# Performance work log

Measured on AMD Instinct MI355X. Metric: run time of the kernel, lower is better.

## Reference

```python
import jax, jax.numpy as jnp
import numpy as np

N = 50000          # total nodes
N_USER = 40000     # main (user) nodes
E = 400000         # edges per node kind
K = 3              # node kinds (separate graphs)
H = 4              # attention heads
F_IN = 128         # n_units[0]
F_OUT = 64         # n_units[1]
NB_CLASSES = 40
SLOPE = 0.2        # leaky relu negative slope


def setup_inputs() -> dict:
    key = jax.random.key(0)
    ks = jax.random.split(key, 12)
    h = jax.random.normal(ks[0], (N, F_IN), dtype=jnp.float32)
    edge_index = jax.random.randint(ks[1], (K, 2, E), 0, N, dtype=jnp.int32)
    # per-kind SpGATLayer params (bias=False)
    w = jax.random.normal(ks[2], (K, H, F_IN, F_OUT), dtype=jnp.float32) * 0.1
    a_src = jax.random.normal(ks[3], (K, H, F_OUT), dtype=jnp.float32) * 0.1
    a_trg = jax.random.normal(ks[4], (K, H, F_OUT), dtype=jnp.float32) * 0.1
    # AdditiveAttention: w1 (d=F_IN -> d2=F_OUT), w2 (d1=F_OUT -> d2=F_OUT), m (d2 -> 1)
    w1 = jax.random.normal(ks[5], (F_IN, F_OUT), dtype=jnp.float32) * 0.1
    w2 = jax.random.normal(ks[6], (F_OUT, F_OUT), dtype=jnp.float32) * 0.1
    m = jax.random.normal(ks[7], (F_OUT,), dtype=jnp.float32) * 0.1
    # final fc: in = F_OUT*(K+1)
    fc_w = jax.random.normal(ks[8], (F_OUT * (K + 1), NB_CLASSES), dtype=jnp.float32) * 0.1
    fc_b = jnp.zeros((NB_CLASSES,), dtype=jnp.float32)
    return {"h": h, "edge_index": edge_index, "w": w, "a_src": a_src,
            "a_trg": a_trg, "w1": w1, "w2": w2, "m": m,
            "fc_w": fc_w, "fc_b": fc_b}


def _spgat_kind(h, src, trg, wk, ask, atk):
    # h: [N, F_IN], wk: [H, F_IN, F_OUT], ask/atk: [H, F_OUT]
    hp = jnp.einsum('nd,hdf->nhf', h, wk)               # [N, H, F_OUT]
    s = jnp.einsum('nhf,hf->nh', hp, ask)               # [N, H]
    t = jnp.einsum('nhf,hf->nh', hp, atk)               # [N, H]
    e = s[src] + t[trg]                                 # [E, H]
    e = jnp.where(e >= 0, e, SLOPE * e)                 # leaky relu
    e = e - jnp.max(e)                                  # global max shift (as in source)
    exp_e = jnp.exp(e)
    denom = jax.ops.segment_sum(exp_e, trg, num_segments=N)  # [N, H]
    alpha = exp_e / (denom[trg] + 1e-16)                # [E, H]
    msg = hp[src] * alpha[:, :, None]                   # [E, H, F_OUT]
    out = jax.ops.segment_sum(msg, trg, num_segments=N) # [N, H, F_OUT]
    return out.mean(axis=1)                             # [N, F_OUT] (last layer head-mean)


def reference(h, edge_index, w, a_src, a_trg, w1, w2, m, fc_w, fc_b):
    heter = []
    for k in range(K):  # fixed small loop over node kinds
        x = _spgat_kind(h, edge_index[k, 0], edge_index[k, 1],
                        w[k], a_src[k], a_trg[k])
        heter.append(x[:N_USER])
    type_aware = jnp.stack(heter, axis=1)               # [N_USER, K, F_OUT]
    feature = h[:N_USER]                                # [N_USER, F_IN]
    q = jnp.tanh((feature @ w1)[:, None, :] + type_aware @ w2)  # [N_USER, K, F_OUT]
    scores = q @ m                                      # [N_USER, K]
    beta = jax.nn.softmax(scores, axis=-1)
    fusion = jnp.einsum('nk,nkf->nf', beta, type_aware) # [N_USER, F_OUT]
    ret = jnp.concatenate([type_aware, fusion[:, None, :]], axis=1)
    ret = ret.reshape(N_USER, -1)                       # [N_USER, F_OUT*(K+1)]
    logits = ret @ fc_w + fc_b
    return jax.nn.log_softmax(logits, axis=-1)
```

## Files before the change

### kernel.cpp

```cpp
#include <hip/hip_runtime.h>
#include <hip/hip_bf16.h>

#define NN    50000
#define NUSER 40000
#define EE    400000
#define KKIND 3
#define HHEAD 4
#define FIN   128
#define FOUT  64
#define NCLS  40

typedef __attribute__((ext_vector_type(8))) short short8;
typedef __attribute__((ext_vector_type(4))) float floatx4;

__device__ __forceinline__ float bf2f(unsigned short u) {
    unsigned int v = ((unsigned int)u) << 16;
    return __uint_as_float(v);
}
__device__ __forceinline__ unsigned short f2bf(float f) {
    unsigned int u = __float_as_uint(f);
    unsigned int r = (u + 0x7FFFu + ((u >> 16) & 1u)) >> 16;
    return (unsigned short)r;
}

#define OFF_H    0
#define OFF_W    6400000
#define OFF_ASRC 6498304
#define OFF_ATRG 6499072
#define OFF_W1   6499840
#define OFF_W2   6508032
#define OFF_M    6512128
#define OFF_FCW  6512192
#define OFF_FCB  6522432
#define CONV_TOT 6522472

__global__ __launch_bounds__(256) void detect_kernel(const unsigned short* __restrict__ hraw,
                                                     int* __restrict__ flag)
{
    __shared__ int cnt;
    if (threadIdx.x == 0) cnt = 0;
    __syncthreads();
    int local = 0;
#pragma unroll
    for (int j = 0; j < 8; j++) {
        unsigned short u = hraw[threadIdx.x * 8 + j];
        int ex = (u >> 7) & 0xFF;
        if (ex >= 0x90) local++;
    }
    atomicAdd(&cnt, local);
    __syncthreads();
    if (threadIdx.x == 0) *flag = (cnt > 100) ? 1 : 0;
}

__global__ __launch_bounds__(256) void conv_kernel(const void* __restrict__ p0, const void* __restrict__ p2,
                                                   const void* __restrict__ p3, const void* __restrict__ p4,
                                                   const void* __restrict__ p5, const void* __restrict__ p6,
                                                   const void* __restrict__ p7, const void* __restrict__ p8,
                                                   const void* __restrict__ p9,
                                                   const int* __restrict__ flagp,
                                                   unsigned short* __restrict__ dst)
{
    int tid = (blockIdx.x * 256 + threadIdx.x) * 8;
    if (tid >= CONV_TOT) return;
    const void* src; int li;
    if      (tid < OFF_W)    { src = p0; li = tid - OFF_H; }
    else if (tid < OFF_ASRC) { src = p2; li = tid - OFF_W; }
    else if (tid < OFF_ATRG) { src = p3; li = tid - OFF_ASRC; }
    else if (tid < OFF_W1)   { src = p4; li = tid - OFF_ATRG; }
    else if (tid < OFF_W2)   { src = p5; li = tid - OFF_W1; }
    else if (tid < OFF_M)    { src = p6; li = tid - OFF_W2; }
    else if (tid < OFF_FCW)  { src = p7; li = tid - OFF_M; }
    else if (tid < OFF_FCB)  { src = p8; li = tid - OFF_FCW; }
    else                     { src = p9; li = tid - OFF_FCB; }
    if (*flagp) {
        const float* fp = (const float*)src + li;
        float4 x = *(const float4*)fp;
        float4 y = *(const float4*)(fp + 4);
        uint4 o;
        o.x = (unsigned int)f2bf(x.x) | ((unsigned int)f2bf(x.y) << 16);
        o.y = (unsigned int)f2bf(x.z) | ((unsigned int)f2bf(x.w) << 16);
        o.z = (unsigned int)f2bf(y.x) | ((unsigned int)f2bf(y.y) << 16);
        o.w = (unsigned int)f2bf(y.z) | ((unsigned int)f2bf(y.w) << 16);
        *(uint4*)(dst + tid) = o;
    } else {
        *(uint4*)(dst + tid) = *(const uint4*)((const unsigned short*)src + li);
    }
}

__global__ __launch_bounds__(256) void repack_w(const unsigned short* __restrict__ w,
                                                unsigned short* __restrict__ wT)
{
    int tid = blockIdx.x * 256 + threadIdx.x;
    if (tid >= 12288) return;
    int f = tid & 63, g = (tid >> 6) & 15, h = (tid >> 10) & 3, k = tid >> 12;
    const unsigned short* src = w + (size_t)(k * 4 + h) * 8192 + f;
    unsigned short* dst = wT + (size_t)tid * 8;
#pragma unroll
    for (int j = 0; j < 8; j++) dst[j] = src[(size_t)(g * 8 + j) * 64];
}

__global__ __launch_bounds__(256) void repack_small(const unsigned short* __restrict__ w1,
                                                    const unsigned short* __restrict__ w2,
                                                    const unsigned short* __restrict__ fcw,
                                                    unsigned short* __restrict__ w1T,
                                                    unsigned short* __restrict__ w2T,
                                                    unsigned short* __restrict__ fcwT)
{
    int tid = blockIdx.x * 256 + threadIdx.x;
    if (tid < 1024) {
        int c = tid & 63, g = tid >> 6;
#pragma unroll
        for (int j = 0; j < 8; j++) w1T[(size_t)(g * 64 + c) * 8 + j] = w1[(size_t)(g * 8 + j) * 64 + c];
    } else if (tid < 1536) {
        int t = tid - 1024; int c = t & 63, g = t >> 6;
#pragma unroll
        for (int j = 0; j < 8; j++) w2T[(size_t)(g * 64 + c) * 8 + j] = w2[(size_t)(g * 8 + j) * 64 + c];
    } else if (tid < 3072) {
        int t = tid - 1536; int c = t % 48, g = t / 48;
#pragma unroll
        for (int j = 0; j < 8; j++)
            fcwT[(size_t)(g * 48 + c) * 8 + j] = (c < NCLS) ? fcw[(size_t)(g * 8 + j) * NCLS + c] : (unsigned short)0;
    }
}

__global__ __launch_bounds__(256) void repack_ast(const unsigned short* __restrict__ asrc_all,
                                                  const unsigned short* __restrict__ atrg_all,
                                                  unsigned short* __restrict__ bst)
{
    int tid = blockIdx.x * 256 + threadIdx.x;
    if (tid >= 1536) return;
    int c = tid & 15, g = (tid >> 4) & 31, k = tid >> 9;
    const unsigned short* ask = asrc_all + k * 256;
    const unsigned short* atk = atrg_all + k * 256;
    unsigned short* dst = bst + (size_t)tid * 8;
#pragma unroll
    for (int j = 0; j < 8; j++) {
        int kd = g * 8 + j;
        int f = kd >> 2, hh = kd & 3;
        unsigned short v = 0;
        if (c < 4)      { if (hh == c)     v = ask[c * 64 + f]; }
        else if (c < 8) { if (hh == c - 4) v = atk[(c - 4) * 64 + f]; }
        dst[j] = v;
    }
}

__global__ __launch_bounds__(256) void hist3(const int* __restrict__ ei,
                                             unsigned int* __restrict__ cnt,
                                             unsigned int* __restrict__ rank)
{
    int k = blockIdx.y;
    const int* trg = ei + (size_t)k * 2 * EE + EE;
    unsigned int* ck = cnt + (size_t)k * NUSER;
    unsigned int* rk = rank + (size_t)k * EE;
    int e0 = blockIdx.x * 1024 + threadIdx.x;
    int t[4];
#pragma unroll
    for (int j = 0; j < 4; j++) {
        int e = e0 + j * 256;
        t[j] = (e < EE) ? trg[e] : NUSER;
    }
    unsigned int r[4];
#pragma unroll
    for (int j = 0; j < 4; j++)
        r[j] = (t[j] < NUSER) ? atomicAdd(&ck[t[j]], 1u) : 0u;
#pragma unroll
    for (int j = 0; j < 4; j++) {
        int e = e0 + j * 256;
        if (e < EE && t[j] < NUSER) rk[e] = r[j];
    }
}

#define SCB 20
__global__ __launch_bounds__(256) void scanA(const unsigned int* __restrict__ cnt,
                                             unsigned int* __restrict__ partials)
{
    int k = blockIdx.y, b = blockIdx.x;
    const unsigned int* c = cnt + (size_t)k * NUSER;
    int base = b * 2048 + threadIdx.x * 8;
    unsigned int s = 0;
#pragma unroll
    for (int j = 0; j < 8; j++) { int idx = base + j; if (idx < NUSER) s += c[idx]; }
#pragma unroll
    for (int off = 1; off < 64; off <<= 1) s += __shfl_xor(s, off, 64);
    __shared__ unsigned int wsum[4];
    int lane = threadIdx.x & 63, wid = threadIdx.x >> 6;
    if (lane == 0) wsum[wid] = s;
    __syncthreads();
    if (threadIdx.x == 0) partials[k * SCB + b] = wsum[0] + wsum[1] + wsum[2] + wsum[3];
}

__global__ __launch_bounds__(256) void scanB(unsigned int* __restrict__ partials,
                                             unsigned int* __restrict__ rowptr)
{
    int wid = threadIdx.x >> 6, lane = threadIdx.x & 63;
    if (wid >= KKIND) return;
    unsigned int v = (lane < SCB) ? partials[wid * SCB + lane] : 0u;
    unsigned int inc = v;
#pragma unroll
    for (int off = 1; off < 32; off <<= 1) {
        unsigned int u = __shfl_up(inc, off, 64);
        if (lane >= off) inc += u;
    }
    if (lane < SCB) partials[wid * SCB + lane] = inc - v;
    if (lane == SCB - 1) rowptr[(size_t)wid * (NUSER + 1) + NUSER] = inc;
}

__global__ __launch_bounds__(256) void scanC(const unsigned int* __restrict__ cnt,
                                             const unsigned int* __restrict__ partials,
                                             unsigned int* __restrict__ rowptr)
{
    int k = blockIdx.y, b = blockIdx.x;
    const unsigned int* c = cnt + (size_t)k * NUSER;
    unsigned int* rp = rowptr + (size_t)k * (NUSER + 1);
    int lane = threadIdx.x & 63, wid = threadIdx.x >> 6;
    int base = b * 2048 + threadIdx.x * 8;
    unsigned int vals[8]; unsigned int s = 0;
#pragma unroll
    for (int j = 0; j < 8; j++) { int idx = base + j; vals[j] = (idx < NUSER) ? c[idx] : 0u; s += vals[j]; }
    unsigned int inc = s;
#pragma unroll
    for (int off = 1; off < 64; off <<= 1) {
        unsigned int u = __shfl_up(inc, off, 64);
        if (lane >= off) inc += u;
    }
    __shared__ unsigned int wsum[4];
    if (lane == 63) wsum[wid] = inc;
    __syncthreads();
    unsigned int woff = 0;
    for (int i = 0; i < wid; i++) woff += wsum[i];
    unsigned int run = partials[k * SCB + b] + woff + (inc - s);
#pragma unroll
    for (int j = 0; j < 8; j++) {
        int idx = base + j;
        if (idx < NUSER) { rp[idx] = run; run += vals[j]; }
    }
}

__global__ __launch_bounds__(256) void scatter3(const int* __restrict__ ei,
                                                const unsigned int* __restrict__ rowptr,
                                                const unsigned int* __restrict__ rank,
                                                int* __restrict__ srcl)
{
    int k = blockIdx.y;
    const int* srcA = ei + (size_t)k * 2 * EE;
    const int* trg = srcA + EE;
    const unsigned int* rp = rowptr + (size_t)k * (NUSER + 1);
    const unsigned int* rk = rank + (size_t)k * EE;
    int* sl = srcl + (size_t)k * EE;
    int e0 = blockIdx.x * 1024 + threadIdx.x;
    int t[4], s[4]; unsigned int r[4];
#pragma unroll
    for (int j = 0; j < 4; j++) {
        int e = e0 + j * 256;
        t[j] = (e < EE) ? trg[e] : NUSER;
        s[j] = (e < EE) ? srcA[e] : 0;
        r[j] = (e < EE && t[j] < NUSER) ? rk[e] : 0u;
    }
    unsigned int base[4];
#pragma unroll
    for (int j = 0; j < 4; j++) base[j] = (t[j] < NUSER) ? rp[t[j]] : 0u;
#pragma unroll
    for (int j = 0; j < 4; j++) {
        int e = e0 + j * 256;
        if (e < EE && t[j] < NUSER) sl[base[j] + r[j]] = s[j];
    }
}

__global__ __launch_bounds__(256) void hp_gemm3(const unsigned short* __restrict__ h,
                                                const unsigned short* __restrict__ wTall,
                                                unsigned short* __restrict__ hp2,
                                                long long hp2_stride, int kbeg, int kcnt)
{
    int q = threadIdx.x >> 6;
    int lane = threadIdx.x & 63;
    int m0 = blockIdx.x * 16;
    int mi = lane & 15, quad = lane >> 4;

    short8 a[4];
    const unsigned short* hrow = h + (size_t)(m0 + mi) * FIN + quad * 8;
#pragma unroll
    for (int kk = 0; kk < 4; kk++) a[kk] = *(const short8*)(hrow + kk * 32);

    int fc = q * 16 + mi;
    for (int kq = 0; kq < kcnt; kq++) {
        const unsigned short* wTk = wTall + (size_t)(kbeg + kq) * 32768;
        unsigned short* hp2k = hp2 + (size_t)kq * hp2_stride;
        floatx4 acc4[4];
#pragma unroll
        for (int hh = 0; hh < 4; hh++) {
            floatx4 acc = {0.f, 0.f, 0.f, 0.f};
#pragma unroll
            for (int kk = 0; kk < 4; kk++) {
                short8 b = *(const short8*)(wTk + (size_t)((hh * 16 + kk * 4 + quad) * 64 + fc) * 8);
                acc = __builtin_amdgcn_mfma_f32_16x16x32_bf16(a[kk], b, acc, 0, 0, 0);
            }
            acc4[hh] = acc;
        }
#pragma unroll
        for (int reg = 0; reg < 4; reg++) {
            ushort4 pk;
            pk.x = f2bf(acc4[0][reg]); pk.y = f2bf(acc4[1][reg]);
            pk.z = f2bf(acc4[2][reg]); pk.w = f2bf(acc4[3][reg]);
            int row = m0 + quad * 4 + reg;
            *(ushort4*)(hp2k + (size_t)row * 256 + fc * 4) = pk;
        }
    }
}

__global__ __launch_bounds__(256) void st_gemm(const unsigned short* __restrict__ hp2,
                                               long long hp2_stride,
                                               const unsigned short* __restrict__ bst,
                                               float* __restrict__ sb, float* __restrict__ tb,
                                               int kbeg)
{
    int kq = blockIdx.y, k = kbeg + kq;
    const unsigned short* hp2k = hp2 + (size_t)kq * hp2_stride;
    const unsigned short* bk = bst + (size_t)k * 4096;
    float* sbk = sb + (size_t)k * NN * 4;
    float* tbk = tb + (size_t)k * NN * 4;

    int wave = threadIdx.x >> 6;
    int lane = threadIdx.x & 63;
    int m0 = (blockIdx.x * 4 + wave) * 16;
    if (m0 >= NN) return;
    int mi = lane & 15, quad = lane >> 4;

    floatx4 acc = {0.f, 0.f, 0.f, 0.f};
#pragma unroll
    for (int kk = 0; kk < 8; kk++) {
        short8 a = *(const short8*)(hp2k + (size_t)(m0 + mi) * 256 + kk * 32 + quad * 8);
        short8 b = *(const short8*)(bk + (size_t)((kk * 4 + quad) * 16 + mi) * 8);
        acc = __builtin_amdgcn_mfma_f32_16x16x32_bf16(a, b, acc, 0, 0, 0);
    }
    if (mi < 8) {
#pragma unroll
        for (int reg = 0; reg < 4; reg++) {
            int n = m0 + quad * 4 + reg;
            if (mi < 4) sbk[n * 4 + mi] = acc[reg];
            else        tbk[n * 4 + (mi - 4)] = acc[reg];
        }
    }
}

__global__ __launch_bounds__(256) void passB_multi(const unsigned int* __restrict__ rowptr_all,
                                                   const int* __restrict__ srcl_all,
                                                   const float* __restrict__ sb,
                                                   const float* __restrict__ tb,
                                                   const unsigned short* __restrict__ hp2,
                                                   long long hp2_stride,
                                                   unsigned short* __restrict__ ret, int kbeg)
{
    __shared__ int    lds_src[4][64];
    __shared__ float4 lds_ew[4][64];
    int kq = blockIdx.y, k = kbeg + kq;
    const unsigned int* rowptr = rowptr_all + (size_t)k * (NUSER + 1);
    const int* srcl = srcl_all + (size_t)k * EE;
    const float* sbk = sb + (size_t)k * NN * 4;
    const float* tbk = tb + (size_t)k * NN * 4;
    const unsigned short* hp2k = hp2 + (size_t)kq * hp2_stride;

    int wid = threadIdx.x >> 6;
    int n = __builtin_amdgcn_readfirstlane(blockIdx.x * 4 + wid);
    int f = threadIdx.x & 63;
    unsigned int beg = rowptr[n], end = rowptr[n + 1];
    float4 t4 = *(const float4*)(tbk + (size_t)n * 4);
    float num0 = 0.f, num1 = 0.f, num2 = 0.f, num3 = 0.f;
    float den0 = 0.f, den1 = 0.f, den2 = 0.f, den3 = 0.f;

    for (unsigned int p0 = beg; p0 < end; p0 += 64) {
        unsigned int cnt = end - p0; if (cnt > 64) cnt = 64;
        int s = 0;
        float4 e = {0.f, 0.f, 0.f, 0.f};
        if ((unsigned int)f < cnt) {
            s = srcl[p0 + f];
            float4 sv = *(const float4*)(sbk + (size_t)s * 4);
            float v0 = sv.x + t4.x, v1 = sv.y + t4.y, v2 = sv.z + t4.z, v3 = sv.w + t4.w;
            v0 = (v0 >= 0.f) ? v0 : 0.2f * v0;  v1 = (v1 >= 0.f) ? v1 : 0.2f * v1;
            v2 = (v2 >= 0.f) ? v2 : 0.2f * v2;  v3 = (v3 >= 0.f) ? v3 : 0.2f * v3;
            e.x = __expf(v0); e.y = __expf(v1); e.z = __expf(v2); e.w = __expf(v3);
        }
        lds_src[wid][f] = s;
        lds_ew[wid][f] = e;
        float d0 = e.x, d1 = e.y, d2 = e.z, d3 = e.w;
#pragma unroll
        for (int off = 1; off < 64; off <<= 1) {
            d0 += __shfl_xor(d0, off, 64); d1 += __shfl_xor(d1, off, 64);
            d2 += __shfl_xor(d2, off, 64); d3 += __shfl_xor(d3, off, 64);
        }
        den0 += d0; den1 += d1; den2 += d2; den3 += d3;
        unsigned int jmax = (cnt + 7u) & ~7u;
        for (unsigned int j = 0; j < jmax; j += 8) {
            int ss[8]; float4 ee[8];
#pragma unroll
            for (int u = 0; u < 8; u++) { ss[u] = lds_src[wid][j + u]; ee[u] = lds_ew[wid][j + u]; }
            ushort4 hv[8];
#pragma unroll
            for (int u = 0; u < 8; u++) hv[u] = *(const ushort4*)(hp2k + (size_t)ss[u] * 256 + f * 4);
#pragma unroll
            for (int u = 0; u < 8; u++) {
                num0 += ee[u].x * bf2f(hv[u].x); num1 += ee[u].y * bf2f(hv[u].y);
                num2 += ee[u].z * bf2f(hv[u].z); num3 += ee[u].w * bf2f(hv[u].w);
            }
        }
    }
    float r = 0.25f * (num0 / (den0 + 1e-16f) + num1 / (den1 + 1e-16f)
                     + num2 / (den2 + 1e-16f) + num3 / (den3 + 1e-16f));
    ret[(size_t)n * 256 + k * 64 + f] = f2bf(r);
}

__global__ __launch_bounds__(256) void qscore_fc(const unsigned short* __restrict__ h,
                                                 const unsigned short* __restrict__ w1T,
                                                 const unsigned short* __restrict__ retA,
                                                 const unsigned short* __restrict__ w2T,
                                                 const unsigned short* __restrict__ mvec,
                                                 const unsigned short* __restrict__ fcwT,
                                                 const unsigned short* __restrict__ bias,
                                                 const int* __restrict__ flagp,
                                                 void* __restrict__ out, int M)
{
    int wave = (blockIdx.x * 256 + threadIdx.x) >> 6;
    int lane = threadIdx.x & 63;
    int m0 = wave * 16;
    if (m0 >= M) return;
    int mi = lane & 15, quad = lane >> 4;

    floatx4 fw[4];
#pragma unroll
    for (int nt = 0; nt < 4; nt++) fw[nt] = (floatx4){0.f, 0.f, 0.f, 0.f};
#pragma unroll
    for (int kk = 0; kk < 4; kk++) {
        short8 a = *(const short8*)(h + (size_t)(m0 + mi) * FIN + kk * 32 + quad * 8);
#pragma unroll
        for (int nt = 0; nt < 4; nt++) {
            short8 b = *(const short8*)(w1T + (size_t)((kk * 4 + quad) * 64 + nt * 16 + mi) * 8);
            fw[nt] = __builtin_amdgcn_mfma_f32_16x16x32_bf16(a, b, fw[nt], 0, 0, 0);
        }
    }

    float pk[3][4];
    short8 afr[3][2];
    for (int k = 0; k < KKIND; k++) {
        floatx4 acc[4];
#pragma unroll
        for (int nt = 0; nt < 4; nt++) acc[nt] = (floatx4){0.f, 0.f, 0.f, 0.f};
#pragma unroll
        for (int kk = 0; kk < 2; kk++) {
            short8 a = *(const short8*)(retA + (size_t)(m0 + mi) * 256 + k * 64 + kk * 32 + quad * 8);
            afr[k][kk] = a;
#pragma unroll
            for (int nt = 0; nt < 4; nt++) {
                short8 b = *(const short8*)(w2T + (size_t)((kk * 4 + quad) * 64 + nt * 16 + mi) * 8);
                acc[nt] = __builtin_amdgcn_mfma_f32_16x16x32_bf16(a, b, acc[nt], 0, 0, 0);
            }
        }
        float part[4] = {0.f, 0.f, 0.f, 0.f};
#pragma unroll
        for (int nt = 0; nt < 4; nt++) {
            int col = nt * 16 + mi;
            float mval = bf2f(mvec[col]);
#pragma unroll
            for (int reg = 0; reg < 4; reg++) {
                float x = acc[nt][reg] + fw[nt][reg];
                float q = 1.f - 2.f / (1.f + __expf(2.f * x));
                part[reg] += q * mval;
            }
        }
#pragma unroll
        for (int off = 1; off < 16; off <<= 1)
#pragma unroll
            for (int reg = 0; reg < 4; reg++) part[reg] += __shfl_xor(part[reg], off, 64);
#pragma unroll
        for (int reg = 0; reg < 4; reg++) pk[k][reg] = part[reg];
    }

    int rsel = mi & 3;
    float sv0 = (rsel == 0) ? pk[0][0] : (rsel == 1) ? pk[0][1] : (rsel == 2) ? pk[0][2] : pk[0][3];
    float sv1 = (rsel == 0) ? pk[1][0] : (rsel == 1) ? pk[1][1] : (rsel == 2) ? pk[1][2] : pk[1][3];
    float sv2 = (rsel == 0) ? pk[2][0] : (rsel == 1) ? pk[2][1] : (rsel == 2) ? pk[2][2] : pk[2][3];
    int srcLane = ((mi >> 2) << 4) | mi;
    float s0 = __shfl(sv0, srcLane, 64);
    float s1 = __shfl(sv1, srcLane, 64);
    float s2 = __shfl(sv2, srcLane, 64);
    float mx0 = fmaxf(s0, fmaxf(s1, s2));
    float e0 = __expf(s0 - mx0), e1 = __expf(s1 - mx0), e2 = __expf(s2 - mx0);
    float inv = 1.f / (e0 + e1 + e2);
    float w0 = e0 * inv, w1 = e1 * inv, w2 = e2 * inv;

    short8 ffr[2];
#pragma unroll
    for (int kk = 0; kk < 2; kk++)
#pragma unroll
        for (int j = 0; j < 8; j++) {
            float fu = w0 * bf2f((unsigned short)afr[0][kk][j])
                     + w1 * bf2f((unsigned short)afr[1][kk][j])
                     + w2 * bf2f((unsigned short)afr[2][kk][j]);
            ffr[kk][j] = (short)f2bf(fu);
        }

    floatx4 acc[3];
#pragma unroll
    for (int nt = 0; nt < 3; nt++) acc[nt] = (floatx4){0.f, 0.f, 0.f, 0.f};
#pragma unroll
    for (int kp = 0; kp < 8; kp++) {
        short8 a = (kp < 6) ? afr[kp >> 1][kp & 1] : ffr[kp - 6];
#pragma unroll
        for (int nt = 0; nt < 3; nt++) {
            short8 b = *(const short8*)(fcwT + (size_t)((kp * 4 + quad) * 48 + nt * 16 + mi) * 8);
            acc[nt] = __builtin_amdgcn_mfma_f32_16x16x32_bf16(a, b, acc[nt], 0, 0, 0);
        }
    }
    int fl = *flagp;
    float bv[3]; bool ok[3];
#pragma unroll
    for (int nt = 0; nt < 3; nt++) {
        int col = nt * 16 + mi;
        ok[nt] = (col < NCLS);
        bv[nt] = ok[nt] ? bf2f(bias[col]) : 0.f;
    }
#pragma unroll
    for (int reg = 0; reg < 4; reg++) {
        float v[3];
#pragma unroll
        for (int nt = 0; nt < 3; nt++)
            v[nt] = ok[nt] ? (acc[nt][reg] + bv[nt]) : -3.4e38f;
        float mx = fmaxf(fmaxf(v[0], v[1]), v[2]);
#pragma unroll
        for (int off = 1; off < 16; off <<= 1) mx = fmaxf(mx, __shfl_xor(mx, off, 64));
        float s = 0.f;
#pragma unroll
        for (int nt = 0; nt < 3; nt++) s += ok[nt] ? __expf(v[nt] - mx) : 0.f;
#pragma unroll
        for (int off = 1; off < 16; off <<= 1) s += __shfl_xor(s, off, 64);
        float lse = mx + __logf(s);
        int row = m0 + quad * 4 + reg;
#pragma unroll
        for (int nt = 0; nt < 3; nt++) {
            int col = nt * 16 + mi;
            if (col < NCLS) {
                float ls = v[nt] - lse;
                size_t idx = (size_t)row * NCLS + col;
                if (fl) ((float*)out)[idx] = ls;
                else    ((unsigned short*)out)[idx] = f2bf(ls);
            }
        }
    }
}

extern "C" void kernel_launch(void* const* d_in, const int* in_sizes, int n_in,
                              void* d_out, int out_size, void* d_ws, size_t ws_size,
                              hipStream_t stream)
{
    (void)in_sizes; (void)n_in; (void)out_size;
    const int* ei = (const int*)d_in[1];

    char* ws = (char*)d_ws;
    unsigned short* conv = (unsigned short*)ws;
    unsigned short* hc   = conv + OFF_H;
    unsigned short* wc   = conv + OFF_W;
    unsigned short* asrc = conv + OFF_ASRC;
    unsigned short* atrg = conv + OFF_ATRG;
    unsigned short* w1c  = conv + OFF_W1;
    unsigned short* w2c  = conv + OFF_W2;
    unsigned short* mc   = conv + OFF_M;
    unsigned short* fcwc = conv + OFF_FCW;
    unsigned short* fcbc = conv + OFF_FCB;
    int* flag             = (int*)(ws + 13044944);
    unsigned short* wT    = (unsigned short*)(ws + 13045248);
    unsigned short* w1T   = (unsigned short*)(ws + 13241856);
    unsigned short* w2T   = (unsigned short*)(ws + 13258240);
    unsigned short* fcwT  = (unsigned short*)(ws + 13266432);
    unsigned short* bst   = (unsigned short*)(ws + 13291008);
    unsigned int* partials= (unsigned int*)(ws + 13315584);
    unsigned int* cnt     = (unsigned int*)(ws + 13315840);
    unsigned int* rowptr  = (unsigned int*)(ws + 13795840);
    int* srcl             = (int*)(ws + 14276096);
    unsigned int* rank    = (unsigned int*)(ws + 19076096);
    float* sbuf           = (float*)(ws + 23876096);
    float* tbuf           = (float*)(ws + 26276096);
    unsigned short* ret   = (unsigned short*)(ws + 28676096);
    unsigned short* hp2   = (unsigned short*)(ws + 49156096);

    const size_t NEED_BIG = 49156096ull + 3ull * NN * 256 * 2;
    int big = (ws_size >= NEED_BIG) ? 1 : 0;

    detect_kernel<<<1, 256, 0, stream>>>((const unsigned short*)d_in[0], flag);
    conv_kernel<<<(CONV_TOT / 8 + 255) / 256, 256, 0, stream>>>(
        d_in[0], d_in[2], d_in[3], d_in[4], d_in[5], d_in[6], d_in[7], d_in[8], d_in[9],
        flag, conv);

    repack_w<<<48, 256, 0, stream>>>(wc, wT);
    repack_small<<<12, 256, 0, stream>>>(w1c, w2c, fcwc, w1T, w2T, fcwT);
    repack_ast<<<6, 256, 0, stream>>>(asrc, atrg, bst);

    hipMemsetAsync(cnt, 0, (size_t)KKIND * NUSER * 4, stream);
    hist3<<<dim3((EE + 1023) / 1024, 3), 256, 0, stream>>>(ei, cnt, rank);
    scanA<<<dim3(SCB, 3), 256, 0, stream>>>(cnt, partials);
    scanB<<<1, 256, 0, stream>>>(partials, rowptr);
    scanC<<<dim3(SCB, 3), 256, 0, stream>>>(cnt, partials, rowptr);
    scatter3<<<dim3((EE + 1023) / 1024, 3), 256, 0, stream>>>(ei, rowptr, rank, srcl);

    if (big) {
        long long stride = (long long)NN * 256;
        hp_gemm3<<<dim3(NN / 16, 1), 256, 0, stream>>>(hc, wT, hp2, stride, 0, 3);
        st_gemm<<<dim3((NN / 16 + 3) / 4, 3), 256, 0, stream>>>(hp2, stride, bst, sbuf, tbuf, 0);
        for (int k = 0; k < KKIND; k++)
            passB_multi<<<dim3(NUSER / 4, 1), 256, 0, stream>>>(rowptr, srcl, sbuf, tbuf,
                                                                hp2 + (size_t)k * stride, 0, ret, k);
    } else {
        for (int k = 0; k < KKIND; k++) {
            hp_gemm3<<<dim3(NN / 16, 1), 256, 0, stream>>>(hc, wT, hp2, 0, k, 1);
            st_gemm<<<dim3((NN / 16 + 3) / 4, 1), 256, 0, stream>>>(hp2, 0, bst, sbuf, tbuf, k);
            passB_multi<<<dim3(NUSER / 4, 1), 256, 0, stream>>>(rowptr, srcl, sbuf, tbuf,
                                                                hp2, 0, ret, k);
        }
    }

    qscore_fc<<<625, 256, 0, stream>>>(hc, w1T, ret, w2T, mc, fcwT, fcbc, flag, d_out, NUSER);
}
```

Baseline: 330.5 us.

## Replace global-atomic CSR histogram with chunked LDS histograms plus per-chunk prefix

Builds the per-target edge histogram with 32 edge chunks per kind and target-half, using packed 16-bit counters in shared memory instead of global atomics. A new scanD kernel prefix-sums the per-chunk counts and writes the totals, and scatter adds the chunk offset to the local rank. This removes contended global atomics and the memset. In exchange it adds a kernel, a larger workspace, strided blkcnt writes, and each histogram block reads its whole chunk twice, once per target half.

```diff
diff --git a/kernel.cpp b/kernel.cpp
--- a/kernel.cpp
+++ b/kernel.cpp
@@ -9,6 +9,11 @@
 #define FIN   128
 #define FOUT  64
 #define NCLS  40
+
+#define CHK  32
+#define CHE  (EE / CHK)
+#define HALF 20000
+#define HWRD 10000
 
 typedef __attribute__((ext_vector_type(8))) short short8;
 typedef __attribute__((ext_vector_type(4))) float floatx4;
@@ -144,30 +149,54 @@
     }
 }
 
-__global__ __launch_bounds__(256) void hist3(const int* __restrict__ ei,
-                                             unsigned int* __restrict__ cnt,
+__global__ __launch_bounds__(256) void histL(const int* __restrict__ ei,
+                                             unsigned int* __restrict__ blkcnt,
                                              unsigned int* __restrict__ rank)
 {
-    int k = blockIdx.y;
+    __shared__ unsigned int lcnt[HWRD];
+    int b = blockIdx.x;
+    int hf = blockIdx.y & 1, k = blockIdx.y >> 1;
     const int* trg = ei + (size_t)k * 2 * EE + EE;
-    unsigned int* ck = cnt + (size_t)k * NUSER;
     unsigned int* rk = rank + (size_t)k * EE;
-    int e0 = blockIdx.x * 1024 + threadIdx.x;
-    int t[4];
-#pragma unroll
-    for (int j = 0; j < 4; j++) {
-        int e = e0 + j * 256;
-        t[j] = (e < EE) ? trg[e] : NUSER;
-    }
-    unsigned int r[4];
-#pragma unroll
-    for (int j = 0; j < 4; j++)
-        r[j] = (t[j] < NUSER) ? atomicAdd(&ck[t[j]], 1u) : 0u;
-#pragma unroll
-    for (int j = 0; j < 4; j++) {
-        int e = e0 + j * 256;
-        if (e < EE && t[j] < NUSER) rk[e] = r[j];
-    }
+    for (int i = threadIdx.x; i < HWRD; i += 256) lcnt[i] = 0u;
+    __syncthreads();
+    int base = b * CHE;
+    int tbase = hf * HALF;
+    for (int i = threadIdx.x; i < CHE; i += 256) {
+        int e = base + i;
+        int tn = trg[e];
+        unsigned int lt = (unsigned int)(tn - tbase);
+        if (lt < HALF) {
+            unsigned int sh = (lt & 1u) * 16u;
+            unsigned int old = atomicAdd(&lcnt[lt >> 1], 1u << sh);
+            rk[e] = (old >> sh) & 0xFFFFu;
+        }
+    }
+    __syncthreads();
+    unsigned int* dst = blkcnt + ((size_t)(k * 2 + hf) * HWRD) * CHK + b;
+    for (int w = threadIdx.x; w < HWRD; w += 256)
+        dst[(size_t)w * CHK] = lcnt[w];
+}
+
+__global__ __launch_bounds__(256) void scanD(unsigned int* __restrict__ blkcnt,
+                                             unsigned int* __restrict__ cnt)
+{
+    int tid = blockIdx.x * 256 + threadIdx.x;
+    if (tid >= KKIND * 2 * HWRD) return;
+    int w = tid % HWRD;
+    int kh = tid / HWRD;
+    int hf = kh & 1, k = kh >> 1;
+    unsigned int* p = blkcnt + (size_t)tid * CHK;
+    unsigned int run = 0;
+#pragma unroll 8
+    for (int b = 0; b < CHK; b++) {
+        unsigned int v = p[b];
+        p[b] = run;
+        run += v;
+    }
+    int t = hf * HALF + w * 2;
+    cnt[(size_t)k * NUSER + t]     = run & 0xFFFFu;
+    cnt[(size_t)k * NUSER + t + 1] = run >> 16;
 }
 
 #define SCB 20
@@ -238,6 +267,7 @@
 
 __global__ __launch_bounds__(256) void scatter3(const int* __restrict__ ei,
                                                 const unsigned int* __restrict__ rowptr,
+                                                const unsigned int* __restrict__ blkpos,
                                                 const unsigned int* __restrict__ rank,
                                                 int* __restrict__ srcl)
 {
@@ -248,21 +278,18 @@
     const unsigned int* rk = rank + (size_t)k * EE;
     int* sl = srcl + (size_t)k * EE;
     int e0 = blockIdx.x * 1024 + threadIdx.x;
-    int t[4], s[4]; unsigned int r[4];
 #pragma unroll
     for (int j = 0; j < 4; j++) {
         int e = e0 + j * 256;
-        t[j] = (e < EE) ? trg[e] : NUSER;
-        s[j] = (e < EE) ? srcA[e] : 0;
-        r[j] = (e < EE && t[j] < NUSER) ? rk[e] : 0u;
-    }
-    unsigned int base[4];
-#pragma unroll
-    for (int j = 0; j < 4; j++) base[j] = (t[j] < NUSER) ? rp[t[j]] : 0u;
-#pragma unroll
-    for (int j = 0; j < 4; j++) {
-        int e = e0 + j * 256;
-        if (e < EE && t[j] < NUSER) sl[base[j] + r[j]] = s[j];
+        if (e >= EE) continue;
+        int tn = trg[e];
+        if (tn >= NUSER) continue;
+        int hf = (tn >= HALF) ? 1 : 0;
+        int lt = tn - hf * HALF;
+        int b = e / CHE;
+        unsigned int pos = blkpos[((size_t)(k * 2 + hf) * HWRD + (lt >> 1)) * CHK + b];
+        pos = (pos >> ((lt & 1) * 16)) & 0xFFFFu;
+        sl[rp[tn] + pos + rk[e]] = srcA[e];
     }
 }
 
@@ -578,9 +605,10 @@
     float* sbuf           = (float*)(ws + 23876096);
     float* tbuf           = (float*)(ws + 26276096);
     unsigned short* ret   = (unsigned short*)(ws + 28676096);
-    unsigned short* hp2   = (unsigned short*)(ws + 49156096);
-
-    const size_t NEED_BIG = 49156096ull + 3ull * NN * 256 * 2;
+    unsigned int* blkcnt  = (unsigned int*)(ws + 49156096);
+    unsigned short* hp2   = (unsigned short*)(ws + 56836096);
+
+    const size_t NEED_BIG = 56836096ull + 3ull * NN * 256 * 2;
     int big = (ws_size >= NEED_BIG) ? 1 : 0;
 
     detect_kernel<<<1, 256, 0, stream>>>((const unsigned short*)d_in[0], flag);
@@ -592,12 +620,12 @@
     repack_small<<<12, 256, 0, stream>>>(w1c, w2c, fcwc, w1T, w2T, fcwT);
     repack_ast<<<6, 256, 0, stream>>>(asrc, atrg, bst);
 
-    hipMemsetAsync(cnt, 0, (size_t)KKIND * NUSER * 4, stream);
-    hist3<<<dim3((EE + 1023) / 1024, 3), 256, 0, stream>>>(ei, cnt, rank);
+    histL<<<dim3(CHK, 2 * KKIND), 256, 0, stream>>>(ei, blkcnt, rank);
+    scanD<<<(KKIND * 2 * HWRD + 255) / 256, 256, 0, stream>>>(blkcnt, cnt);
     scanA<<<dim3(SCB, 3), 256, 0, stream>>>(cnt, partials);
     scanB<<<1, 256, 0, stream>>>(partials, rowptr);
     scanC<<<dim3(SCB, 3), 256, 0, stream>>>(cnt, partials, rowptr);
-    scatter3<<<dim3((EE + 1023) / 1024, 3), 256, 0, stream>>>(ei, rowptr, rank, srcl);
+    scatter3<<<dim3((EE + 1023) / 1024, 3), 256, 0, stream>>>(ei, rowptr, blkcnt, rank, srcl);
 
     if (big) {
         long long stride = (long long)NN * 256;
```

Measured after the change: 363.6 us. 10.0% more time.
